# Kernel tuning notes

Measured on AMD Instinct MI355X. Metric: run time of the kernel, lower is better.

## Reference

```python
import jax, jax.numpy as jnp
import numpy as np

N = 50000      # nodes
E = 800000     # edges (avg degree 16)
D_IN = 369     # input feature dim
D = 128        # output_dim / GGNN hidden
T = 13         # max_edge_types
STEPS = 8      # GRU propagation steps
G = 256        # graphs in batch


def setup_inputs() -> dict:
    key = jax.random.key(0)
    ks = jax.random.split(key, 13)
    s = 0.05
    return {
        "x": jax.random.normal(ks[0], (N, D_IN), jnp.float32),
        "edge_index": jax.random.randint(ks[1], (2, E), 0, N, dtype=jnp.int64),
        "edge_attr": jax.random.randint(ks[2], (E,), 0, T, dtype=jnp.int64),
        "batch": jnp.sort(jax.random.randint(ks[3], (N,), 0, G, dtype=jnp.int64)),
        "lin_w": jax.random.normal(ks[4], (D_IN, D), jnp.float32) * s,
        "lin_b": jax.random.normal(ks[5], (D,), jnp.float32) * s,
        # per-edge-type GatedGraphConv: weight[t, step] is [D, D]
        "ggnn_w": jax.random.normal(ks[6], (T, STEPS, D, D), jnp.float32) * s,
        # per-edge-type GRUCell params (torch layout: [3*D, D] rows = r,z,n)
        "gru_w_ih": jax.random.normal(ks[7], (T, 3 * D, D), jnp.float32) * s,
        "gru_w_hh": jax.random.normal(ks[8], (T, 3 * D, D), jnp.float32) * s,
        "gru_b_ih": jax.random.normal(ks[9], (T, 3 * D), jnp.float32) * s,
        "gru_b_hh": jax.random.normal(ks[10], (T, 3 * D), jnp.float32) * s,
        "cls_w": jax.random.normal(ks[11], (D, 2), jnp.float32) * s,
        "cls_b": jax.random.normal(ks[12], (2,), jnp.float32) * s,
    }


def reference(x, edge_index, edge_attr, batch,
              lin_w, lin_b, ggnn_w, gru_w_ih, gru_w_hh, gru_b_ih, gru_b_hh,
              cls_w, cls_b):
    n_nodes = x.shape[0]
    h0 = x @ lin_w + lin_b                     # [N, D]; dropout omitted (eval)
    src, dst = edge_index[0], edge_index[1]

    messages = jnp.zeros_like(h0)
    for t in range(T):                          # fixed small set of edge types
        emask = (edge_attr == t).astype(h0.dtype)   # [E] select edges of this type
        w_ih, w_hh = gru_w_ih[t], gru_w_hh[t]
        b_ih, b_hh = gru_b_ih[t], gru_b_hh[t]

        def step(h, w):
            # message passing: aggregate (h @ w)[src] at dst over type-t edges
            xw = h @ w                           # [N, D]
            m = jax.ops.segment_sum(xw[src] * emask[:, None], dst,
                                    num_segments=n_nodes)
            # GRUCell(m, h)
            gi = m @ w_ih.T + b_ih               # [N, 3D]
            gh = h @ w_hh.T + b_hh
            ir, iz, i_n = jnp.split(gi, 3, axis=-1)
            hr, hz, h_n = jnp.split(gh, 3, axis=-1)
            r = jax.nn.sigmoid(ir + hr)
            z = jax.nn.sigmoid(iz + hz)
            n = jnp.tanh(i_n + r * h_n)
            return (1.0 - z) * n + z * h, None

        h_t, _ = jax.lax.scan(step, h0, ggnn_w[t])   # 8 steps
        messages = messages + h_t

    # global_mean_pool over graphs
    sums = jax.ops.segment_sum(messages, batch, num_segments=G)   # [G, D]
    counts = jax.ops.segment_sum(jnp.ones((n_nodes,), messages.dtype), batch,
                                 num_segments=G)
    pooled = sums / jnp.maximum(counts, 1.0)[:, None]
    return pooled @ cls_w + cls_b                                 # [G, 2]
```

## Files before the change

kernel.cpp:

```cpp
#include <hip/hip_runtime.h>
#include <hip/hip_bf16.h>
#include <stdint.h>

typedef __attribute__((ext_vector_type(8))) short   short8;
typedef __attribute__((ext_vector_type(8))) __bf16  bf16x8;
typedef __attribute__((ext_vector_type(4))) float   f32x4;

#define DEV __device__ __forceinline__

DEV float bf2f(uint16_t u){ union{uint32_t i; float f;} v; v.i = ((uint32_t)u)<<16; return v.f; }
DEV uint16_t f2bf(float f){
  union{ __hip_bfloat16 b; uint16_t u; } v; v.b = __float2bfloat16(f); return v.u;
}
DEV float sigmf(float x){ return 1.0f/(1.0f + __expf(-x)); }
DEV float tanhx(float x){ x = fminf(15.f, fmaxf(-15.f, x)); float e = __expf(-2.0f*x);
  return (1.0f-e)/(1.0f+e); }

DEV bf16x8 as_bf(short8 s){ union{ short8 s; bf16x8 b; } u; u.s = s; return u.b; }
DEV f32x4 mfma16(short8 a, short8 b, f32x4 c){
  return __builtin_amdgcn_mfma_f32_16x16x32_bf16(as_bf(a), as_bf(b), c, 0, 0, 0);
}
DEV f32x4 vzero(){ f32x4 v; v[0]=0.f; v[1]=0.f; v[2]=0.f; v[3]=0.f; return v; }

__global__ void cast_bf16_kernel(const float* __restrict__ in, uint16_t* __restrict__ out, int n){
  int i = blockIdx.x*256 + threadIdx.x;
  if (i < n) out[i] = f2bf(in[i]);
}

__global__ void cast_swz_kernel(const float* __restrict__ in, uint16_t* __restrict__ out, int n){
  int i = blockIdx.x*256 + threadIdx.x;
  if (i < n){
    int k = i & 127, row = i >> 7;
    out[(row<<7) + (((k>>3) ^ (row&15))<<3) + (k&7)] = f2bf(in[i]);
  }
}

__global__ void xpad_kernel(const float* __restrict__ x, uint16_t* __restrict__ xb, int rows){
  int i = blockIdx.x*256 + threadIdx.x;
  if (i < rows*384){
    int r = i/384, c = i - r*384;
    xb[i] = (c < 369) ? f2bf(x[r*369 + c]) : (uint16_t)0;
  }
}

__global__ void lwt_kernel(const float* __restrict__ lw, uint16_t* __restrict__ lwT){
  int i = blockIdx.x*256 + threadIdx.x;
  if (i < 128*384){
    int nn = i/384, k = i - nn*384;
    lwT[i] = (k < 369) ? f2bf(lw[k*128 + nn]) : (uint16_t)0;
  }
}

__global__ __launch_bounds__(256,2)
void gemm_bt_kernel(const uint16_t* __restrict__ A, const uint16_t* __restrict__ B,
                    uint16_t* __restrict__ C,
                    int lda, int ldb, int M, int K4,
                    const float* __restrict__ bias, int swz,
                    long sA, long sB, long sC, int divA)
{
  int by = blockIdx.y;
  A += (long)(by/divA)*sA; B += (long)by*sB; C += (long)by*sC;
  int tid = threadIdx.x, lane = tid&63, wave = tid>>6;
  int l15 = lane&15, quad = lane>>4;
  int m0 = blockIdx.x*64 + wave*16;
  f32x4 acc[8];
  #pragma unroll
  for (int nf=0; nf<8; ++nf) acc[nf] = vzero();
  int mrow = min(m0 + l15, M-1);
  const char* arow = (const char*)(A + (long)mrow*lda) + quad*16;
  for (int kk=0; kk<K4; ++kk){
    short8 a = *(const short8*)(arow + kk*64);
    #pragma unroll
    for (int nf=0; nf<8; ++nf){
      const char* brow = (const char*)(B + (long)(nf*16+l15)*ldb) + quad*16;
      short8 b = *(const short8*)(brow + kk*64);
      acc[nf] = mfma16(a, b, acc[nf]);
    }
  }
  #pragma unroll
  for (int nf=0; nf<8; ++nf){
    int col = nf*16 + l15;
    float bb = bias ? bias[col] : 0.0f;
    #pragma unroll
    for (int i=0; i<4; ++i){
      int row = m0 + quad*4 + i;
      if (row < M){
        float v = acc[nf][i] + bb;
        int idx = swz ? (row*128 + (((col>>3)^(row&15))<<3) + (col&7)) : (row*128+col);
        C[idx] = f2bf(v);
      }
    }
  }
}

__global__ void edge_count_kernel(const int* __restrict__ ei, const int* __restrict__ ea,
                                  int* __restrict__ cnt, int E, int n){
  int e = blockIdx.x*256 + threadIdx.x;
  if (e < E){
    int dst = ei[E + e];
    int t = ea[e];
    atomicAdd(&cnt[t*n + dst], 1);
  }
}

__global__ void csr_alloc_kernel(const int* __restrict__ cnt, int* __restrict__ row_start,
                                 int* __restrict__ cursor, int* __restrict__ total, int R){
  __shared__ int wsum[4];
  __shared__ int base;
  int i = blockIdx.x*256 + threadIdx.x;
  int c = (i < R) ? cnt[i] : 0;
  int lane = threadIdx.x & 63, wave = threadIdx.x >> 6;
  int x = c;
  #pragma unroll
  for (int d=1; d<64; d<<=1){ int y = __shfl_up(x, d, 64); if (lane >= d) x += y; }
  if (lane == 63) wsum[wave] = x;
  __syncthreads();
  if (threadIdx.x == 0){
    int s0=wsum[0], s1=wsum[1], s2=wsum[2], s3=wsum[3];
    base = atomicAdd(total, s0+s1+s2+s3);
    wsum[0]=0; wsum[1]=s0; wsum[2]=s0+s1; wsum[3]=s0+s1+s2;
  }
  __syncthreads();
  int st = base + wsum[wave] + (x - c);
  if (i < R){ row_start[i] = st; cursor[i] = st; }
}

__global__ void edge_fill_kernel(const int* __restrict__ ei, const int* __restrict__ ea,
                                 int* __restrict__ cursor, int* __restrict__ csr, int E, int n){
  int e = blockIdx.x*256 + threadIdx.x;
  if (e < E){
    int src = ei[e], dst = ei[E+e], t = ea[e];
    int pos = atomicAdd(&cursor[t*n + dst], 1);
    csr[pos] = src;
  }
}

__global__ void agg_kernel(const uint16_t* __restrict__ h_in_b,
                           uint16_t* __restrict__ agg_b,
                           const int* __restrict__ row_start_b,
                           const int* __restrict__ row_cnt_b,
                           const int* __restrict__ csr_src,
                           int n, int t_off, long hin_stride)
{
  const int t = t_off + blockIdx.y;
  const uint16_t* h_in = h_in_b + (long)blockIdx.y*hin_stride;
  uint16_t* agg = agg_b + (long)blockIdx.y*((long)n*128);
  int id = blockIdx.x*256 + threadIdx.x;
  int row = id >> 4, c = (id & 15) * 8;
  if (row < n){
    int st = row_start_b[(size_t)t*n + row];
    int cn = row_cnt_b  [(size_t)t*n + row];
    float acc[8] = {0,0,0,0,0,0,0,0};
    for (int e=0; e<cn; ++e){
      int src = csr_src[st + e];
      short8 v = *(const short8*)(h_in + (long)src*128 + c);
      #pragma unroll
      for (int j=0; j<8; ++j) acc[j] += bf2f((uint16_t)v[j]);
    }
    short8 pk;
    #pragma unroll
    for (int j=0; j<8; ++j) pk[j] = (short)f2bf(acc[j]);
    *(short8*)(agg + (long)row*128 + c) = pk;
  }
}

__global__ __launch_bounds__(256, 2)
void ggnn_step_kernel(const uint16_t* __restrict__ h_in_b,
                      const uint16_t* __restrict__ agg_b,
                      uint16_t* __restrict__ h_out_b,
                      const uint16_t* __restrict__ W1_b,
                      const uint16_t* __restrict__ W2_b,
                      const float* __restrict__ bih_b,
                      const float* __restrict__ bhh_b,
                      int n, int s, int t_off,
                      long hin_stride, long hstride)
{
  __shared__ __align__(16) uint16_t sB[128*128];
  const int t = t_off + blockIdx.y;
  const uint16_t* h_in = h_in_b + (long)blockIdx.y*hin_stride;
  const uint16_t* agg  = agg_b  + (long)blockIdx.y*hstride;
  uint16_t*       h_out= h_out_b+ (long)blockIdx.y*hstride;
  const uint16_t* W1s = W1_b + (size_t)(t*8+s)*384*128;
  const uint16_t* W2s = W2_b + (size_t)t*384*128;
  const float* bih = bih_b + t*384;
  const float* bhh = bhh_b + t*384;

  const int tid = threadIdx.x, lane = tid&63, wave = tid>>6;
  const int l15 = lane&15, quad = lane>>4;
  const int rbase = blockIdx.x*64;
  const int ar = rbase + wave*16 + l15;
  const int arc = min(ar, n-1);

  const uint16_t* stp[6] = { W1s, W2s, W1s+2*16384, W2s+2*16384, W1s+16384, W2s+16384 };

  short8 tmp[8];
  {
    const char* g = (const char*)stp[0] + tid*16;
    #pragma unroll
    for (int it=0; it<8; ++it) tmp[it] = *(const short8*)(g + it*4096);
  }

  short8 hfr[4], afr[4];
  {
    const short8* hrow = (const short8*)(h_in + (long)arc*128);
    const short8* arow = (const short8*)(agg  + (long)arc*128);
    #pragma unroll
    for (int kk=0; kk<4; ++kk){ hfr[kk] = hrow[kk*4 + quad]; afr[kk] = arow[kk*4 + quad]; }
  }

  auto mma = [&](f32x4* a8, const short8* frag){
    #pragma unroll
    for (int kk=0; kk<4; ++kk){
      int ch = ((kk*4+quad)^l15)<<4;
      short8 a = frag[kk];
      #pragma unroll
      for (int nf=0; nf<8; ++nf){
        short8 b = *(const short8*)((const char*)sB + (nf*16+l15)*256 + ch);
        a8[nf] = mfma16(a, b, a8[nf]);
      }
    }
  };

  f32x4 rg[8], nng[8], zg[8];
  #pragma unroll
  for (int nf=0; nf<8; ++nf){ rg[nf]=vzero(); nng[nf]=vzero(); zg[nf]=vzero(); }

  #pragma unroll
  for (int g=0; g<6; ++g){
    __syncthreads();
    {
      char* l = (char*)sB + tid*16;
      #pragma unroll
      for (int it=0; it<8; ++it) *(short8*)(l + it*4096) = tmp[it];
    }
    __syncthreads();
    if (g < 5){
      const char* gp = (const char*)stp[g+1] + tid*16;
      #pragma unroll
      for (int it=0; it<8; ++it) tmp[it] = *(const short8*)(gp + it*4096);
    }
    if (g == 0)      mma(rg, afr);
    else if (g == 1){
      mma(rg, hfr);
      #pragma unroll
      for (int nf=0; nf<8; ++nf){
        int col = nf*16 + l15;
        float bs = bih[col] + bhh[col];
        #pragma unroll
        for (int i=0; i<4; ++i) rg[nf][i] = sigmf(rg[nf][i] + bs);
      }
    }
    else if (g == 2) mma(nng, afr);
    else if (g == 3){
      f32x4 nh[8];
      #pragma unroll
      for (int nf=0; nf<8; ++nf) nh[nf] = vzero();
      mma(nh, hfr);
      #pragma unroll
      for (int nf=0; nf<8; ++nf){
        int col = nf*16 + l15;
        float bin = bih[256+col], bhn = bhh[256+col];
        #pragma unroll
        for (int i=0; i<4; ++i)
          nng[nf][i] = tanhx(nng[nf][i] + bin + rg[nf][i]*(nh[nf][i] + bhn));
      }
    }
    else if (g == 4) mma(zg, afr);
    else             mma(zg, hfr);
  }

  #pragma unroll
  for (int nf=0; nf<8; ++nf){
    int col = nf*16 + l15;
    float bs = bih[128+col] + bhh[128+col];
    #pragma unroll
    for (int i=0; i<4; ++i){
      int row = rbase + wave*16 + quad*4 + i;
      if (row < n){
        float z = sigmf(zg[nf][i] + bs);
        float hv = bf2f(h_in[(long)row*128 + col]);
        float hnew = nng[nf][i] + z*(hv - nng[nf][i]);
        h_out[(long)row*128 + col] = f2bf(hnew);
      }
    }
  }
}

__global__ void reduce_kernel(const uint16_t* __restrict__ hfin, float* __restrict__ messages,
                              long stride, int nt, int accumulate, int total8){
  int i = blockIdx.x*256 + threadIdx.x;
  if (i < total8){
    float acc[8];
    #pragma unroll
    for (int j=0;j<8;++j) acc[j] = 0.f;
    if (accumulate){
      #pragma unroll
      for (int j=0;j<8;++j) acc[j] = messages[(long)i*8 + j];
    }
    for (int t=0; t<nt; ++t){
      short8 v = *(const short8*)(hfin + (long)t*stride + (long)i*8);
      #pragma unroll
      for (int j=0;j<8;++j) acc[j] += bf2f((uint16_t)v[j]);
    }
    #pragma unroll
    for (int j=0;j<8;++j) messages[(long)i*8 + j] = acc[j];
  }
}

__global__ void pool_kernel(const float* __restrict__ messages, const int* __restrict__ batch,
                            float* __restrict__ sums, int* __restrict__ cntg, int n){
  int id = blockIdx.x*256 + threadIdx.x;
  int col = id & 127;
  int nb = (id >> 7) * 8;
  float acc = 0.f; int curg = -1; int ccount = 0;
  for (int j=0; j<8; ++j){
    int node = nb + j;
    if (node < n){
      int g = batch[node];
      if (g != curg){
        if (curg >= 0){
          atomicAdd(&sums[curg*128+col], acc);
          if (col == 0) atomicAdd(&cntg[curg], ccount);
        }
        curg = g; acc = 0.f; ccount = 0;
      }
      acc += messages[(long)node*128 + col];
      ccount++;
    }
  }
  if (curg >= 0){
    atomicAdd(&sums[curg*128+col], acc);
    if (col == 0) atomicAdd(&cntg[curg], ccount);
  }
}

__global__ void classify_kernel(const float* __restrict__ sums, const int* __restrict__ cntg,
                                const float* __restrict__ cls_w, const float* __restrict__ cls_b,
                                float* __restrict__ out, int G){
  int g = threadIdx.x;
  if (g < G){
    float inv = 1.0f / fmaxf((float)cntg[g], 1.0f);
    float o0 = 0.f, o1 = 0.f;
    for (int d=0; d<128; ++d){
      float p = sums[g*128+d]*inv;
      o0 += p*cls_w[d*2];
      o1 += p*cls_w[d*2+1];
    }
    out[g*2]   = o0 + cls_b[0];
    out[g*2+1] = o1 + cls_b[1];
  }
}

extern "C" void kernel_launch(void* const* d_in, const int* in_sizes, int n_in,
                              void* d_out, int out_size, void* d_ws, size_t ws_size,
                              hipStream_t stream)
{
  const float* x      = (const float*)d_in[0];
  const int*   ei     = (const int*)d_in[1];
  const int*   ea     = (const int*)d_in[2];
  const int*   batch  = (const int*)d_in[3];
  const float* lin_w  = (const float*)d_in[4];
  const float* lin_b  = (const float*)d_in[5];
  const float* ggnn_w = (const float*)d_in[6];
  const float* w_ih   = (const float*)d_in[7];
  const float* w_hh   = (const float*)d_in[8];
  const float* b_ih   = (const float*)d_in[9];
  const float* b_hh   = (const float*)d_in[10];
  const float* cls_w  = (const float*)d_in[11];
  const float* cls_b  = (const float*)d_in[12];
  float* out = (float*)d_out;

  const int N = in_sizes[3];
  const int E = in_sizes[2];
  const int T = in_sizes[9] / 384;
  const int G = out_size / 2;
  const int STEPS = 8;

  struct Layout {
    float *messages, *sums; int *cntg, *total;
    int *cnt, *row_start, *csr;
    uint16_t *W2t, *W1t, *h0;
    uint16_t *hT, *agg;
    int *cursor; uint16_t *xb, *lwT, *gwb, *wihb;
    size_t zero_off, zero_len, end;
  };
  auto make_layout = [&](int nh)->Layout{
    Layout L; char* base = (char*)d_ws; char* p = base;
    auto A = [&](size_t b)->char*{ char* r = p; p += (b + 255) & ~(size_t)255; return r; };
    L.messages  = (float*)A((size_t)N*128*4);
    char* z0 = p;
    L.sums      = (float*)A((size_t)G*128*4);
    L.cntg      = (int*)  A((size_t)G*4);
    L.total     = (int*)  A(256);
    L.zero_off = (size_t)(z0 - base); L.zero_len = (size_t)(p - z0);
    L.cnt       = (int*)  A((size_t)T*N*4);
    L.row_start = (int*)  A((size_t)T*N*4);
    L.csr       = (int*)  A((size_t)E*4);
    L.W2t       = (uint16_t*)A((size_t)T*384*128*2);
    L.W1t       = (uint16_t*)A((size_t)T*8*384*128*2);
    L.h0        = (uint16_t*)A((size_t)N*128*2);
    char* R = p;
    size_t hb  = (size_t)N*128*2;
    size_t hba = ((size_t)nh*hb + 255) & ~(size_t)255;
    L.hT = (uint16_t*)R; L.agg = (uint16_t*)(R + hba);
    size_t hreg = 2*hba;
    char* q = R;
    auto B = [&](size_t b)->char*{ char* r = q; q += (b + 255) & ~(size_t)255; return r; };
    L.cursor = (int*)     B((size_t)T*N*4);
    L.xb     = (uint16_t*)B((size_t)N*384*2);
    L.lwT    = (uint16_t*)B((size_t)128*384*2);
    L.gwb    = (uint16_t*)B((size_t)T*8*128*128*2);
    L.wihb   = (uint16_t*)B((size_t)T*384*128*2);
    size_t preg = (size_t)(q - R);
    L.end = (size_t)(R - base) + (hreg > preg ? hreg : preg);
    return L;
  };
  int nh = 1;
  { int cand[6] = {7, 6, 5, 4, 3, 2};
    for (int i=0; i<6; ++i){
      int c = cand[i] < T ? cand[i] : T;
      if (make_layout(c).end <= ws_size){ nh = c; break; }
    } }
  Layout L = make_layout(nh);

  hipMemsetAsync((char*)d_ws + L.zero_off, 0, L.zero_len, stream);
  hipMemsetAsync(L.cnt, 0, (size_t)T*N*4, stream);

  const int ngw = T*8*128*128, nwih = T*384*128;
  cast_bf16_kernel<<<(ngw+255)/256, 256, 0, stream>>>(ggnn_w, L.gwb, ngw);
  cast_bf16_kernel<<<(nwih+255)/256, 256, 0, stream>>>(w_ih, L.wihb, nwih);
  cast_swz_kernel <<<(nwih+255)/256, 256, 0, stream>>>(w_hh, L.W2t, nwih);
  xpad_kernel<<<((N*384)+255)/256, 256, 0, stream>>>(x, L.xb, N);
  lwt_kernel<<<(128*384+255)/256, 256, 0, stream>>>(lin_w, L.lwT);

  gemm_bt_kernel<<<dim3(6, T*8), 256, 0, stream>>>(L.wihb, L.gwb, L.W1t, 128, 128, 384, 4,
      nullptr, 1, (long)384*128, (long)128*128, (long)384*128, 8);
  gemm_bt_kernel<<<dim3((N+63)/64, 1), 256, 0, stream>>>(L.xb, L.lwT, L.h0, 384, 384, N, 12,
      lin_b, 0, 0, 0, 0, 1);

  edge_count_kernel<<<(E+255)/256, 256, 0, stream>>>(ei, ea, L.cnt, E, N);
  csr_alloc_kernel <<<(T*N+255)/256, 256, 0, stream>>>(L.cnt, L.row_start, L.cursor, L.total, T*N);
  edge_fill_kernel <<<(E+255)/256, 256, 0, stream>>>(ei, ea, L.cursor, L.csr, E, N);

  const int nblk = (N+63)/64;
  const int ablk = (N*16 + 255)/256;
  const long hs = (long)N*128;
  const int total8 = N*128/8;
  const int ngroups = (T + nh - 1)/nh;

  for (int gidx=0; gidx<ngroups; ++gidx){
    int t0 = gidx*nh, nt = (T - t0 < nh) ? (T - t0) : nh;
    for (int s=0; s<STEPS; ++s){
      const uint16_t* hin = (s==0) ? L.h0 : L.hT;
      long hin_stride = (s==0) ? 0 : hs;
      agg_kernel<<<dim3(ablk, nt), 256, 0, stream>>>(
          hin, L.agg, L.row_start, L.cnt, L.csr, N, t0, hin_stride);
      ggnn_step_kernel<<<dim3(nblk, nt), 256, 0, stream>>>(
          hin, L.agg, L.hT, L.W1t, L.W2t, b_ih, b_hh,
          N, s, t0, hin_stride, hs);
    }
    reduce_kernel<<<(total8+255)/256, 256, 0, stream>>>(L.hT, L.messages, hs, nt,
                                                        (gidx>0) ? 1 : 0, total8);
  }

  pool_kernel<<<((N*128)+2047)/2048, 256, 0, stream>>>(L.messages, batch, L.sums, L.cntg, N);
  classify_kernel<<<1, 256, 0, stream>>>(L.sums, L.cntg, cls_w, cls_b, out, G);
}
```

Before: 3.461 ms.

## Double-buffer GRU weight tiles via direct global-to-LDS loads and 2x2 wave tiling

The GGNN step kernel now streams each 128x128 weight block straight into LDS with global_load_lds into a double buffer, replacing the register-staged copy and one of the two barriers per block. Waves are regrouped 2x2 so each computes 32 rows by 64 columns, halving B-fragment LDS reads per MFMA. The gate order is changed so the n-gate and z-gate accumulators share registers, which lowers register pressure. The cost is doubled LDS use (64KB), which may reduce how many blocks fit per CU, plus reliance on hand-placed vmcnt waits.

```diff
diff --git a/kernel.cpp b/kernel.cpp
--- a/kernel.cpp
+++ b/kernel.cpp
@@ -21,6 +21,11 @@
   return __builtin_amdgcn_mfma_f32_16x16x32_bf16(as_bf(a), as_bf(b), c, 0, 0, 0);
 }
 DEV f32x4 vzero(){ f32x4 v; v[0]=0.f; v[1]=0.f; v[2]=0.f; v[3]=0.f; return v; }
+
+DEV void gload16(const uint16_t* g, uint16_t* l){
+  __builtin_amdgcn_global_load_lds((const __attribute__((address_space(1))) void*)g,
+                                   (__attribute__((address_space(3))) void*)l, 16, 0, 0);
+}
 
 __global__ void cast_bf16_kernel(const float* __restrict__ in, uint16_t* __restrict__ out, int n){
   int i = blockIdx.x*256 + threadIdx.x;
@@ -175,7 +180,7 @@
                       int n, int s, int t_off,
                       long hin_stride, long hstride)
 {
-  __shared__ __align__(16) uint16_t sB[128*128];
+  __shared__ __align__(16) uint16_t sB[2][128*128];
   const int t = t_off + blockIdx.y;
   const uint16_t* h_in = h_in_b + (long)blockIdx.y*hin_stride;
   const uint16_t* agg  = agg_b  + (long)blockIdx.y*hstride;
@@ -187,103 +192,128 @@
 
   const int tid = threadIdx.x, lane = tid&63, wave = tid>>6;
   const int l15 = lane&15, quad = lane>>4;
+  const int wr = wave>>1, wc = wave&1;
   const int rbase = blockIdx.x*64;
-  const int ar = rbase + wave*16 + l15;
-  const int arc = min(ar, n-1);
-
-  const uint16_t* stp[6] = { W1s, W2s, W1s+2*16384, W2s+2*16384, W1s+16384, W2s+16384 };
-
-  short8 tmp[8];
+
+  const uint16_t* stp[6] = { W1s, W2s, W2s+2*16384, W1s+2*16384, W1s+16384, W2s+16384 };
+
   {
-    const char* g = (const char*)stp[0] + tid*16;
-    #pragma unroll
-    for (int it=0; it<8; ++it) tmp[it] = *(const short8*)(g + it*4096);
-  }
-
-  short8 hfr[4], afr[4];
+    const uint16_t* g = stp[0] + tid*8;
+    uint16_t* l = &sB[0][tid*8];
+    #pragma unroll
+    for (int it=0; it<8; ++it) gload16(g + it*2048, l + it*2048);
+  }
+
+  const int ar0 = min(rbase + wr*32 +      l15, n-1);
+  const int ar1 = min(rbase + wr*32 + 16 + l15, n-1);
+  short8 hfr[2][4], afr[2][4];
   {
-    const short8* hrow = (const short8*)(h_in + (long)arc*128);
-    const short8* arow = (const short8*)(agg  + (long)arc*128);
-    #pragma unroll
-    for (int kk=0; kk<4; ++kk){ hfr[kk] = hrow[kk*4 + quad]; afr[kk] = arow[kk*4 + quad]; }
-  }
-
-  auto mma = [&](f32x4* a8, const short8* frag){
+    const short8* h0 = (const short8*)(h_in + (long)ar0*128);
+    const short8* h1 = (const short8*)(h_in + (long)ar1*128);
+    const short8* a0 = (const short8*)(agg  + (long)ar0*128);
+    const short8* a1 = (const short8*)(agg  + (long)ar1*128);
     #pragma unroll
     for (int kk=0; kk<4; ++kk){
-      int ch = ((kk*4+quad)^l15)<<4;
-      short8 a = frag[kk];
-      #pragma unroll
-      for (int nf=0; nf<8; ++nf){
-        short8 b = *(const short8*)((const char*)sB + (nf*16+l15)*256 + ch);
-        a8[nf] = mfma16(a, b, a8[nf]);
+      hfr[0][kk] = h0[kk*4 + quad]; hfr[1][kk] = h1[kk*4 + quad];
+      afr[0][kk] = a0[kk*4 + quad]; afr[1][kk] = a1[kk*4 + quad];
+    }
+  }
+
+  auto mma = [&](const uint16_t* bufp, f32x4 (&acc)[2][4], const short8 (&frag)[2][4]){
+    const char* base = (const char*)bufp + wc*64*256;
+    #pragma unroll
+    for (int kk=0; kk<4; ++kk){
+      const int ch = ((kk*4+quad)^l15)<<4;
+      #pragma unroll
+      for (int nf=0; nf<4; ++nf){
+        short8 b = *(const short8*)(base + (nf*16+l15)*256 + ch);
+        acc[0][nf] = mfma16(frag[0][kk], b, acc[0][nf]);
+        acc[1][nf] = mfma16(frag[1][kk], b, acc[1][nf]);
       }
     }
   };
 
-  f32x4 rg[8], nng[8], zg[8];
-  #pragma unroll
-  for (int nf=0; nf<8; ++nf){ rg[nf]=vzero(); nng[nf]=vzero(); zg[nf]=vzero(); }
+  f32x4 rg[2][4], nn[2][4];
+  #pragma unroll
+  for (int mi=0; mi<2; ++mi)
+    #pragma unroll
+    for (int nf=0; nf<4; ++nf){ rg[mi][nf]=vzero(); nn[mi][nf]=vzero(); }
 
   #pragma unroll
   for (int g=0; g<6; ++g){
-    __syncthreads();
-    {
-      char* l = (char*)sB + tid*16;
-      #pragma unroll
-      for (int it=0; it<8; ++it) *(short8*)(l + it*4096) = tmp[it];
-    }
-    __syncthreads();
     if (g < 5){
-      const char* gp = (const char*)stp[g+1] + tid*16;
-      #pragma unroll
-      for (int it=0; it<8; ++it) tmp[it] = *(const short8*)(gp + it*4096);
-    }
-    if (g == 0)      mma(rg, afr);
+      const uint16_t* gp = stp[g+1] + tid*8;
+      uint16_t* lp = &sB[(g+1)&1][tid*8];
+      #pragma unroll
+      for (int it=0; it<8; ++it) gload16(gp + it*2048, lp + it*2048);
+      asm volatile("s_waitcnt vmcnt(8)" ::: "memory");
+    } else {
+      asm volatile("s_waitcnt vmcnt(0)" ::: "memory");
+    }
+    __builtin_amdgcn_s_barrier();
+
+    const uint16_t* bufp = sB[g&1];
+    if (g == 0)      mma(bufp, rg, afr);
     else if (g == 1){
-      mma(rg, hfr);
-      #pragma unroll
-      for (int nf=0; nf<8; ++nf){
-        int col = nf*16 + l15;
-        float bs = bih[col] + bhh[col];
+      mma(bufp, rg, hfr);
+      #pragma unroll
+      for (int mi=0; mi<2; ++mi)
         #pragma unroll
-        for (int i=0; i<4; ++i) rg[nf][i] = sigmf(rg[nf][i] + bs);
+        for (int nf=0; nf<4; ++nf){
+          int col = wc*64 + nf*16 + l15;
+          float bs = bih[col] + bhh[col];
+          #pragma unroll
+          for (int i=0; i<4; ++i) rg[mi][nf][i] = sigmf(rg[mi][nf][i] + bs);
+        }
+    }
+    else if (g == 2){
+      mma(bufp, nn, hfr);
+      #pragma unroll
+      for (int mi=0; mi<2; ++mi)
+        #pragma unroll
+        for (int nf=0; nf<4; ++nf){
+          int col = wc*64 + nf*16 + l15;
+          float bin = bih[256+col], bhn = bhh[256+col];
+          #pragma unroll
+          for (int i=0; i<4; ++i){
+            nn[mi][nf][i] = bin + rg[mi][nf][i]*(nn[mi][nf][i] + bhn);
+            rg[mi][nf][i] = 0.f;
+          }
+          rg[mi][nf] = vzero();
+        }
+    }
+    else if (g == 3){
+      mma(bufp, nn, afr);
+      #pragma unroll
+      for (int mi=0; mi<2; ++mi)
+        #pragma unroll
+        for (int nf=0; nf<4; ++nf)
+          #pragma unroll
+          for (int i=0; i<4; ++i) nn[mi][nf][i] = tanhx(nn[mi][nf][i]);
+    }
+    else if (g == 4) mma(bufp, rg, afr);
+    else             mma(bufp, rg, hfr);
+
+    __builtin_amdgcn_s_barrier();
+  }
+
+  #pragma unroll
+  for (int mi=0; mi<2; ++mi)
+    #pragma unroll
+    for (int nf=0; nf<4; ++nf){
+      int col = wc*64 + nf*16 + l15;
+      float bs = bih[128+col] + bhh[128+col];
+      #pragma unroll
+      for (int i=0; i<4; ++i){
+        int row = rbase + wr*32 + mi*16 + quad*4 + i;
+        if (row < n){
+          float z = sigmf(rg[mi][nf][i] + bs);
+          float hv = bf2f(h_in[(long)row*128 + col]);
+          float hnew = nn[mi][nf][i] + z*(hv - nn[mi][nf][i]);
+          h_out[(long)row*128 + col] = f2bf(hnew);
+        }
       }
     }
-    else if (g == 2) mma(nng, afr);
-    else if (g == 3){
-      f32x4 nh[8];
-      #pragma unroll
-      for (int nf=0; nf<8; ++nf) nh[nf] = vzero();
-      mma(nh, hfr);
-      #pragma unroll
-      for (int nf=0; nf<8; ++nf){
-        int col = nf*16 + l15;
-        float bin = bih[256+col], bhn = bhh[256+col];
-        #pragma unroll
-        for (int i=0; i<4; ++i)
-          nng[nf][i] = tanhx(nng[nf][i] + bin + rg[nf][i]*(nh[nf][i] + bhn));
-      }
-    }
-    else if (g == 4) mma(zg, afr);
-    else             mma(zg, hfr);
-  }
-
-  #pragma unroll
-  for (int nf=0; nf<8; ++nf){
-    int col = nf*16 + l15;
-    float bs = bih[128+col] + bhh[128+col];
-    #pragma unroll
-    for (int i=0; i<4; ++i){
-      int row = rbase + wave*16 + quad*4 + i;
-      if (row < n){
-        float z = sigmf(zg[nf][i] + bs);
-        float hv = bf2f(h_in[(long)row*128 + col]);
-        float hnew = nng[nf][i] + z*(hv - nng[nf][i]);
-        h_out[(long)row*128 + col] = f2bf(hnew);
-      }
-    }
-  }
 }
 
 __global__ void reduce_kernel(const uint16_t* __restrict__ hfin, float* __restrict__ messages,
```

New measurement: 3.639 ms. 1.05x slower.

## Double-buffer GRU weight tiles via direct global-to-LDS loads with 512-thread blocks

Applied to the files above, without the earlier changes.

Rewrites the GRU step kernel to load weight tiles straight into a double-buffered LDS array with global_load_lds, so the next tile's load overlaps the current MFMA work instead of staging through registers. Blocks grow to 512 threads covering 128 rows, which amortises each weight tile load over twice as many rows. The gate accumulators are reordered so the n-gate reuses one accumulator and z reuses the r accumulator, cutting register pressure. It uses hand-placed vmcnt waits and barriers, so an ordering mistake could read incomplete LDS data, and the doubled LDS footprint may lower occupancy.

```diff
diff --git a/kernel.cpp b/kernel.cpp
--- a/kernel.cpp
+++ b/kernel.cpp
@@ -21,6 +21,11 @@
   return __builtin_amdgcn_mfma_f32_16x16x32_bf16(as_bf(a), as_bf(b), c, 0, 0, 0);
 }
 DEV f32x4 vzero(){ f32x4 v; v[0]=0.f; v[1]=0.f; v[2]=0.f; v[3]=0.f; return v; }
+
+DEV void gload16(const uint16_t* g, uint16_t* l){
+  __builtin_amdgcn_global_load_lds((const __attribute__((address_space(1))) void*)g,
+                                   (__attribute__((address_space(3))) void*)l, 16, 0, 0);
+}
 
 __global__ void cast_bf16_kernel(const float* __restrict__ in, uint16_t* __restrict__ out, int n){
   int i = blockIdx.x*256 + threadIdx.x;
@@ -164,7 +169,7 @@
   }
 }
 
-__global__ __launch_bounds__(256, 2)
+__global__ __launch_bounds__(512, 4)
 void ggnn_step_kernel(const uint16_t* __restrict__ h_in_b,
                       const uint16_t* __restrict__ agg_b,
                       uint16_t* __restrict__ h_out_b,
@@ -175,7 +180,7 @@
                       int n, int s, int t_off,
                       long hin_stride, long hstride)
 {
-  __shared__ __align__(16) uint16_t sB[128*128];
+  __shared__ __align__(16) uint16_t sB[2][128*128];
   const int t = t_off + blockIdx.y;
   const uint16_t* h_in = h_in_b + (long)blockIdx.y*hin_stride;
   const uint16_t* agg  = agg_b  + (long)blockIdx.y*hstride;
@@ -187,61 +192,62 @@
 
   const int tid = threadIdx.x, lane = tid&63, wave = tid>>6;
   const int l15 = lane&15, quad = lane>>4;
-  const int rbase = blockIdx.x*64;
-  const int ar = rbase + wave*16 + l15;
-  const int arc = min(ar, n-1);
-
-  const uint16_t* stp[6] = { W1s, W2s, W1s+2*16384, W2s+2*16384, W1s+16384, W2s+16384 };
-
-  short8 tmp[8];
+  const int rbase = blockIdx.x*128;
+
+  const uint16_t* stp[6] = { W1s, W2s, W2s+2*16384, W1s+2*16384, W1s+16384, W2s+16384 };
+
   {
-    const char* g = (const char*)stp[0] + tid*16;
-    #pragma unroll
-    for (int it=0; it<8; ++it) tmp[it] = *(const short8*)(g + it*4096);
-  }
-
+    const uint16_t* gp = stp[0] + tid*8;
+    uint16_t* lp = &sB[0][tid*8];
+    #pragma unroll
+    for (int it=0; it<4; ++it) gload16(gp + it*4096, lp + it*4096);
+  }
+
+  const int ar = min(rbase + wave*16 + l15, n-1);
   short8 hfr[4], afr[4];
   {
-    const short8* hrow = (const short8*)(h_in + (long)arc*128);
-    const short8* arow = (const short8*)(agg  + (long)arc*128);
+    const short8* hrow = (const short8*)(h_in + (long)ar*128);
+    const short8* arow = (const short8*)(agg  + (long)ar*128);
     #pragma unroll
     for (int kk=0; kk<4; ++kk){ hfr[kk] = hrow[kk*4 + quad]; afr[kk] = arow[kk*4 + quad]; }
   }
 
-  auto mma = [&](f32x4* a8, const short8* frag){
+  auto mma = [&](const uint16_t* bufp, f32x4 (&acc)[8], const short8 (&frag)[4]){
     #pragma unroll
     for (int kk=0; kk<4; ++kk){
-      int ch = ((kk*4+quad)^l15)<<4;
+      const int ch = ((kk*4+quad)^l15)<<4;
       short8 a = frag[kk];
       #pragma unroll
       for (int nf=0; nf<8; ++nf){
-        short8 b = *(const short8*)((const char*)sB + (nf*16+l15)*256 + ch);
-        a8[nf] = mfma16(a, b, a8[nf]);
+        short8 b = *(const short8*)((const char*)bufp + (nf*16+l15)*256 + ch);
+        acc[nf] = mfma16(a, b, acc[nf]);
       }
     }
   };
 
-  f32x4 rg[8], nng[8], zg[8];
-  #pragma unroll
-  for (int nf=0; nf<8; ++nf){ rg[nf]=vzero(); nng[nf]=vzero(); zg[nf]=vzero(); }
+  f32x4 rg[8], nn[8];
+  #pragma unroll
+  for (int nf=0; nf<8; ++nf){ rg[nf]=vzero(); nn[nf]=vzero(); }
 
   #pragma unroll
   for (int g=0; g<6; ++g){
-    __syncthreads();
-    {
-      char* l = (char*)sB + tid*16;
-      #pragma unroll
-      for (int it=0; it<8; ++it) *(short8*)(l + it*4096) = tmp[it];
-    }
-    __syncthreads();
     if (g < 5){
-      const char* gp = (const char*)stp[g+1] + tid*16;
-      #pragma unroll
-      for (int it=0; it<8; ++it) tmp[it] = *(const short8*)(gp + it*4096);
-    }
-    if (g == 0)      mma(rg, afr);
+      __builtin_amdgcn_sched_barrier(0);
+      const uint16_t* gp = stp[g+1] + tid*8;
+      uint16_t* lp = &sB[(g+1)&1][tid*8];
+      #pragma unroll
+      for (int it=0; it<4; ++it) gload16(gp + it*4096, lp + it*4096);
+      asm volatile("s_waitcnt vmcnt(4)" ::: "memory");
+      __builtin_amdgcn_sched_barrier(0);
+    } else {
+      asm volatile("s_waitcnt vmcnt(0)" ::: "memory");
+    }
+    __builtin_amdgcn_s_barrier();
+
+    const uint16_t* bufp = sB[g&1];
+    if (g == 0)      mma(bufp, rg, afr);
     else if (g == 1){
-      mma(rg, hfr);
+      mma(bufp, rg, hfr);
       #pragma unroll
       for (int nf=0; nf<8; ++nf){
         int col = nf*16 + l15;
@@ -250,23 +256,29 @@
         for (int i=0; i<4; ++i) rg[nf][i] = sigmf(rg[nf][i] + bs);
       }
     }
-    else if (g == 2) mma(nng, afr);
-    else if (g == 3){
-      f32x4 nh[8];
-      #pragma unroll
-      for (int nf=0; nf<8; ++nf) nh[nf] = vzero();
-      mma(nh, hfr);
+    else if (g == 2){
+      mma(bufp, nn, hfr);
       #pragma unroll
       for (int nf=0; nf<8; ++nf){
         int col = nf*16 + l15;
         float bin = bih[256+col], bhn = bhh[256+col];
         #pragma unroll
         for (int i=0; i<4; ++i)
-          nng[nf][i] = tanhx(nng[nf][i] + bin + rg[nf][i]*(nh[nf][i] + bhn));
-      }
-    }
-    else if (g == 4) mma(zg, afr);
-    else             mma(zg, hfr);
+          nn[nf][i] = bin + rg[nf][i]*(nn[nf][i] + bhn);
+        rg[nf] = vzero();
+      }
+    }
+    else if (g == 3){
+      mma(bufp, nn, afr);
+      #pragma unroll
+      for (int nf=0; nf<8; ++nf)
+        #pragma unroll
+        for (int i=0; i<4; ++i) nn[nf][i] = tanhx(nn[nf][i]);
+    }
+    else if (g == 4) mma(bufp, rg, afr);
+    else             mma(bufp, rg, hfr);
+
+    __builtin_amdgcn_s_barrier();
   }
 
   #pragma unroll
@@ -277,9 +289,9 @@
     for (int i=0; i<4; ++i){
       int row = rbase + wave*16 + quad*4 + i;
       if (row < n){
-        float z = sigmf(zg[nf][i] + bs);
+        float z = sigmf(rg[nf][i] + bs);
         float hv = bf2f(h_in[(long)row*128 + col]);
-        float hnew = nng[nf][i] + z*(hv - nng[nf][i]);
+        float hnew = nn[nf][i] + z*(hv - nn[nf][i]);
         h_out[(long)row*128 + col] = f2bf(hnew);
       }
     }
@@ -442,7 +454,7 @@
   csr_alloc_kernel <<<(T*N+255)/256, 256, 0, stream>>>(L.cnt, L.row_start, L.cursor, L.total, T*N);
   edge_fill_kernel <<<(E+255)/256, 256, 0, stream>>>(ei, ea, L.cursor, L.csr, E, N);
 
-  const int nblk = (N+63)/64;
+  const int nblk = (N+127)/128;
   const int ablk = (N*16 + 255)/256;
   const long hs = (long)N*128;
   const int total8 = N*128/8;
@@ -455,7 +467,7 @@
       long hin_stride = (s==0) ? 0 : hs;
       agg_kernel<<<dim3(ablk, nt), 256, 0, stream>>>(
           hin, L.agg, L.row_start, L.cnt, L.csr, N, t0, hin_stride);
-      ggnn_step_kernel<<<dim3(nblk, nt), 256, 0, stream>>>(
+      ggnn_step_kernel<<<dim3(nblk, nt), 512, 0, stream>>>(
           hin, L.agg, L.hT, L.W1t, L.W2t, b_ih, b_hh,
           N, s, t0, hin_stride, hs);
     }
```

New measurement: 3.251 ms, median of 2. 1.06x faster.
